# Performance work log

Hardware: AMD Instinct MI355X
Metric: run time of the kernel (lower is better)

The kernel has to match this reference:

```python
import jax, jax.numpy as jnp
import numpy as np

DIM = 4096  # hadamard_dim, power of 2 -> K=1, pure FWHT with 1/sqrt(n) scaling


def fwht(x):
    """Fast Walsh-Hadamard transform along the last axis, normalized by 1/sqrt(n).

    Butterfly network: log2(n) stages of pairwise add/sub. Matches the math of
    multiplying by the normalized n x n Hadamard matrix (x @ H / sqrt(n)).
    """
    orig_shape = x.shape
    n = orig_shape[-1]
    x = x.reshape(-1, n)
    h = 1
    while h < n:  # static unrolled loop over log2(n) stages (n is static)
        # view as [rows, n/(2h), 2, h]; butterfly pairs are (s=0, s=1)
        xb = x.reshape(-1, n // (2 * h), 2, h)
        a = xb[:, :, 0, :]
        b = xb[:, :, 1, :]
        x = jnp.stack([a + b, a - b], axis=2).reshape(-1, n)
        h *= 2
    scale = jnp.asarray(1.0 / np.sqrt(n), dtype=x.dtype)
    return (x * scale).reshape(orig_shape)


def setup_inputs() -> dict:
    key = jax.random.key(0)
    x = jax.random.normal(key, (4, 2048, DIM), dtype=jnp.float32)
    return {"x": x}


def reference(x):
    # force_fp32=True path: compute in fp32 (x already fp32), cast back to input dtype
    x_dtype = x.dtype
    y = fwht(x.astype(jnp.float32))
    return y.astype(x_dtype)
```

## Files before the change

### kernel.cpp

```cpp
#include <hip/hip_runtime.h>


using v4 = __attribute__((ext_vector_type(4))) float;

__device__ __forceinline__ void had16(float x[16]) {
#pragma unroll
    for (int h = 1; h < 16; h <<= 1) {
#pragma unroll
        for (int i = 0; i < 16; ++i) {
            if (!(i & h)) {
                float a = x[i], b = x[i ^ h];
                x[i] = a + b; x[i ^ h] = a - b;
            }
        }
    }
}

__global__ void __launch_bounds__(256) fwht4096_kernel(const float* __restrict__ in,
                                                       float* __restrict__ out) {
    __shared__ float lds[4096];
    const int t = threadIdx.x;
    const size_t base = (size_t)blockIdx.x * 4096;
    const v4* in4 = reinterpret_cast<const v4*>(in + base);
    v4* out4 = reinterpret_cast<v4*>(out + base);

    v4 v[4];
#pragma unroll
    for (int j = 0; j < 4; ++j) v[j] = __builtin_nontemporal_load(&in4[t + 256 * j]);

#pragma unroll
    for (int j = 0; j < 4; ++j) {
        float a = v[j][0], b = v[j][1], c = v[j][2], d = v[j][3];
        float ab = a + b, amb = a - b, cd = c + d, cmd = c - d;
        v[j][0] = ab + cd; v[j][1] = amb + cmd; v[j][2] = ab - cd; v[j][3] = amb - cmd;
    }
    {
        v4 s0 = v[0] + v[1], d0 = v[0] - v[1];
        v4 s1 = v[2] + v[3], d1 = v[2] - v[3];
        v[0] = s0 + s1; v[2] = s0 - s1;
        v[1] = d0 + d1; v[3] = d0 - d1;
    }
    {
        v4* l4 = reinterpret_cast<v4*>(lds);
        const int wb = t ^ ((t >> 4) & 7);
#pragma unroll
        for (int j = 0; j < 4; ++j) l4[wb + 256 * j] = v[j];
    }
    __syncthreads();

    float x[16];

    {
        const int b2 = (t & 3) + 64 * (t >> 2);
        const int s2 = (t >> 2) & 7;
#pragma unroll
        for (int r = 0; r < 16; ++r) x[r] = lds[b2 + 4 * (r ^ s2)];
        had16(x);
#pragma unroll
        for (int r = 0; r < 16; ++r) lds[b2 + 4 * (r ^ s2)] = x[r];
    }
    __syncthreads();

    {
        const int l = t & 63, w = t >> 6;
        const int b3 = 1024 * w;
#pragma unroll
        for (int r = 0; r < 16; ++r) x[r] = lds[(l ^ ((r & 7) << 2)) + 64 * r + b3];
        had16(x);
        const float scale = 0.015625f;
#pragma unroll
        for (int r = 0; r < 16; ++r) lds[(l ^ ((r & 7) << 2)) + 64 * r + b3] = x[r] * scale;
    }
    __syncthreads();

    {
        const v4* l4 = reinterpret_cast<const v4*>(lds);
        const int wb = t ^ ((t >> 4) & 7);
#pragma unroll
        for (int j = 0; j < 4; ++j) {
            v4 o = l4[wb + 256 * j];
            __builtin_nontemporal_store(o, &out4[t + 256 * j]);
        }
    }
}

extern "C" void kernel_launch(void* const* d_in, const int* in_sizes, int n_in,
                              void* d_out, int out_size, void* d_ws, size_t ws_size,
                              hipStream_t stream) {
    const float* x = (const float*)d_in[0];
    float* out = (float*)d_out;
    const int rows = in_sizes[0] >> 12;
    fwht4096_kernel<<<dim3(rows), dim3(256), 0, stream>>>(x, out);
}
```

Baseline: 218.0 us.

## Use permlane swaps for in-wave butterflies and fuse final stage with store

```diff
diff --git a/kernel.cpp b/kernel.cpp
--- a/kernel.cpp
+++ b/kernel.cpp
@@ -2,6 +2,27 @@
 
 
 using v4 = __attribute__((ext_vector_type(4))) float;
+using u2 = __attribute__((ext_vector_type(2))) unsigned;
+
+__device__ __forceinline__ void bfly_perm32(float& x, float& y) {
+    u2 r = __builtin_amdgcn_permlane32_swap(__float_as_uint(x), __float_as_uint(y),
+                                            false, false);
+    float u = __uint_as_float(r[0]), v = __uint_as_float(r[1]);
+    float s = u + v, d = u - v;
+    u2 r2 = __builtin_amdgcn_permlane32_swap(__float_as_uint(s), __float_as_uint(d),
+                                             false, false);
+    x = __uint_as_float(r2[0]); y = __uint_as_float(r2[1]);
+}
+
+__device__ __forceinline__ void bfly_perm16(float& x, float& y) {
+    u2 r = __builtin_amdgcn_permlane16_swap(__float_as_uint(x), __float_as_uint(y),
+                                            false, false);
+    float u = __uint_as_float(r[0]), v = __uint_as_float(r[1]);
+    float s = u + v, d = u - v;
+    u2 r2 = __builtin_amdgcn_permlane16_swap(__float_as_uint(s), __float_as_uint(d),
+                                             false, false);
+    x = __uint_as_float(r2[0]); y = __uint_as_float(r2[1]);
+}
 
 __device__ __forceinline__ void had16(float x[16]) {
 #pragma unroll
@@ -41,6 +62,15 @@
         v[1] = d0 + d1; v[3] = d0 - d1;
     }
     {
+#pragma unroll
+        for (int e = 0; e < 4; ++e) {
+            float a0 = v[0][e], a1 = v[1][e], a2 = v[2][e], a3 = v[3][e];
+            bfly_perm16(a0, a1); bfly_perm16(a2, a3);
+            bfly_perm32(a0, a1); bfly_perm32(a2, a3);
+            v[0][e] = a0; v[1][e] = a1; v[2][e] = a2; v[3][e] = a3;
+        }
+    }
+    {
         v4* l4 = reinterpret_cast<v4*>(lds);
         const int wb = t ^ ((t >> 4) & 7);
 #pragma unroll
@@ -48,9 +78,8 @@
     }
     __syncthreads();
 
-    float x[16];
-
     {
+        float x[16];
         const int b2 = (t & 3) + 64 * (t >> 2);
         const int s2 = (t >> 2) & 7;
 #pragma unroll
@@ -62,25 +91,26 @@
     __syncthreads();
 
     {
+        const v4* l4 = reinterpret_cast<const v4*>(lds);
         const int l = t & 63, w = t >> 6;
-        const int b3 = 1024 * w;
+        v4 g[4];
 #pragma unroll
-        for (int r = 0; r < 16; ++r) x[r] = lds[(l ^ ((r & 7) << 2)) + 64 * r + b3];
-        had16(x);
+        for (int m = 0; m < 4; ++m) {
+            const int F = l + 64 * m + 256 * w;
+            const int rb = F ^ ((F >> 4) & 7);
+            g[m] = l4[rb];
+        }
+        v4 s0 = g[0] + g[1], d0 = g[0] - g[1];
+        v4 s1 = g[2] + g[3], d1 = g[2] - g[3];
         const float scale = 0.015625f;
-#pragma unroll
-        for (int r = 0; r < 16; ++r) lds[(l ^ ((r & 7) << 2)) + 64 * r + b3] = x[r] * scale;
-    }
-    __syncthreads();
-
-    {
-        const v4* l4 = reinterpret_cast<const v4*>(lds);
-        const int wb = t ^ ((t >> 4) & 7);
-#pragma unroll
-        for (int j = 0; j < 4; ++j) {
-            v4 o = l4[wb + 256 * j];
-            __builtin_nontemporal_store(o, &out4[t + 256 * j]);
-        }
+        v4 o0 = (s0 + s1) * scale;
+        v4 o1 = (d0 + d1) * scale;
+        v4 o2 = (s0 - s1) * scale;
+        v4 o3 = (d0 - d1) * scale;
+        __builtin_nontemporal_store(o0, &out4[l + 256 * w]);
+        __builtin_nontemporal_store(o1, &out4[l + 64 + 256 * w]);
+        __builtin_nontemporal_store(o2, &out4[l + 128 + 256 * w]);
+        __builtin_nontemporal_store(o3, &out4[l + 192 + 256 * w]);
     }
 }
 
```

After: 217.8 us. About the same (-0.1%).
